# Kernel optimization log

Measured on AMD Instinct MI355X. Metric: run time of the kernel, lower is better.

The kernel has to match this reference:

```python
import jax, jax.numpy as jnp
import numpy as np

IN_Q = 256   # in_features // 4
OUT_Q = 256  # out_features // 4


def setup_inputs() -> dict:
    key = jax.random.key(0)
    kx, kr, ki, kj, kk = jax.random.split(key, 5)
    stdv = 1.0 / np.sqrt(IN_Q)
    return {
        "x": jax.random.normal(kx, (4, 8192, IN_Q * 4), dtype=jnp.float32),
        "r_weight": jax.random.uniform(kr, (OUT_Q, IN_Q), minval=-stdv, maxval=stdv, dtype=jnp.float32),
        "i_weight": jax.random.uniform(ki, (OUT_Q, IN_Q), minval=-stdv, maxval=stdv, dtype=jnp.float32),
        "j_weight": jax.random.uniform(kj, (OUT_Q, IN_Q), minval=-stdv, maxval=stdv, dtype=jnp.float32),
        "k_weight": jax.random.uniform(kk, (OUT_Q, IN_Q), minval=-stdv, maxval=stdv, dtype=jnp.float32),
        "bias": jnp.zeros((OUT_Q * 4,), dtype=jnp.float32),
    }


def reference(x, r_weight, i_weight, j_weight, k_weight, bias):
    batch_dims = x.shape[:-1]
    xq = x.reshape(*batch_dims, IN_Q, 4)  # [..., in_q, 4]
    r_x, i_x, j_x, k_x = xq[..., 0], xq[..., 1], xq[..., 2], xq[..., 3]

    lin = lambda v, w: jnp.einsum('...i,oi->...o', v, w)  # F.linear, no bias

    out_r = lin(r_x, r_weight) - lin(i_x, i_weight) - lin(j_x, j_weight) - lin(k_x, k_weight)
    out_i = lin(r_x, i_weight) + lin(i_x, r_weight) + lin(j_x, k_weight) - lin(k_x, j_weight)
    out_j = lin(r_x, j_weight) - lin(i_x, k_weight) + lin(j_x, r_weight) + lin(k_x, i_weight)
    out_k = lin(r_x, k_weight) + lin(i_x, j_weight) - lin(j_x, i_weight) + lin(k_x, r_weight)

    out = jnp.stack([out_r, out_i, out_j, out_k], axis=-1)  # [..., out_q, 4]
    out = out.reshape(*batch_dims, OUT_Q * 4)
    return out + bias
```

## Files before the change

kernel.cpp:

```cpp
#include <hip/hip_runtime.h>


typedef __attribute__((ext_vector_type(8))) short bf16x8;
typedef __attribute__((ext_vector_type(4))) float f32x4;

#define M_TOT 32768
#define N_TOT 1024
#define K_TOT 1024
#define BM 128
#define BN 128
#define BK 32

__device__ __forceinline__ unsigned short f2bf(float f) {
    union { float f; unsigned int u; } v; v.f = f;
    unsigned int u = v.u;
    u += 0x7fffu + ((u >> 16) & 1u);
    return (unsigned short)(u >> 16);
}

__global__ __launch_bounds__(256) void cvt_x(const float4* __restrict__ x,
                                             ushort4* __restrict__ y) {
    int idx = blockIdx.x * 256 + threadIdx.x;
    float4 a = x[idx];
    ushort4 o;
    o.x = f2bf(a.x); o.y = f2bf(a.y); o.z = f2bf(a.z); o.w = f2bf(a.w);
    y[idx] = o;
}

__global__ __launch_bounds__(256) void build_w(const float* __restrict__ R,
                                               const float* __restrict__ I,
                                               const float* __restrict__ J,
                                               const float* __restrict__ Kw,
                                               ushort4* __restrict__ Wb) {
    int n = blockIdx.x;
    int i = threadIdx.x;
    int o = n >> 2, co = n & 3;
    int base = o * 256 + i;
    float r = R[base], ii = I[base], j = J[base], k = Kw[base];
    float v0, v1, v2, v3;
    if (co == 0)      { v0 = r;  v1 = -ii; v2 = -j;  v3 = -k; }
    else if (co == 1) { v0 = ii; v1 = r;   v2 = k;   v3 = -j; }
    else if (co == 2) { v0 = j;  v1 = -k;  v2 = r;   v3 = ii; }
    else              { v0 = k;  v1 = j;   v2 = -ii; v3 = r;  }
    ushort4 w;
    w.x = f2bf(v0); w.y = f2bf(v1); w.z = f2bf(v2); w.w = f2bf(v3);
    Wb[n * 256 + i] = w;
}

__device__ __forceinline__ void async_lds16(const void* g, void* l) {
    __builtin_amdgcn_global_load_lds(
        (const __attribute__((address_space(1))) unsigned int*)g,
        (__attribute__((address_space(3))) unsigned int*)l,
        16, 0, 0);
}

__global__ __launch_bounds__(256) void gemm_bt(
        const unsigned short* __restrict__ A,
        const unsigned short* __restrict__ B,
        const float* __restrict__ bias,
        float* __restrict__ C) {
    __shared__ unsigned short As[BM * BK];
    __shared__ unsigned short Bs[BN * BK];

    const int tid  = threadIdx.x;
    const int wave = tid >> 6;
    const int lane = tid & 63;
    const int quad = lane >> 4;
    const int r16  = lane & 15;
    const int wm   = wave & 1;
    const int wn   = wave >> 1;

    const int m0 = blockIdx.x * BM;
    const int n0 = blockIdx.y * BN;

    f32x4 acc[4][4];
#pragma unroll
    for (int i = 0; i < 4; ++i)
#pragma unroll
        for (int j = 0; j < 4; ++j)
            acc[i][j] = (f32x4){0.f, 0.f, 0.f, 0.f};

    const int srow = lane >> 2;
    const int scol = (lane & 3) * 8;

    for (int k0 = 0; k0 < K_TOT; k0 += BK) {
        __syncthreads();
#pragma unroll
        for (int j = 0; j < 2; ++j) {
            int q   = wave * 2 + j;
            int row = q * 16 + srow;
            async_lds16(A + (size_t)(m0 + row) * K_TOT + k0 + scol, As + q * 512);
            async_lds16(B + (size_t)(n0 + row) * K_TOT + k0 + scol, Bs + q * 512);
        }
        __syncthreads();

        bf16x8 af[4], bf[4];
#pragma unroll
        for (int i = 0; i < 4; ++i) {
            af[i] = *(const bf16x8*)(As + (wm * 64 + i * 16 + r16) * BK + quad * 8);
            bf[i] = *(const bf16x8*)(Bs + (wn * 64 + i * 16 + r16) * BK + quad * 8);
        }
#pragma unroll
        for (int i = 0; i < 4; ++i)
#pragma unroll
            for (int j = 0; j < 4; ++j)
                acc[i][j] = __builtin_amdgcn_mfma_f32_16x16x32_bf16(
                    af[i], bf[j], acc[i][j], 0, 0, 0);
    }

#pragma unroll
    for (int j = 0; j < 4; ++j) {
        int col  = n0 + wn * 64 + j * 16 + r16;
        float bv = bias[col];
#pragma unroll
        for (int i = 0; i < 4; ++i) {
            int rowb = m0 + wm * 64 + i * 16 + quad * 4;
            f32x4 v  = acc[i][j];
#pragma unroll
            for (int r = 0; r < 4; ++r)
                C[(size_t)(rowb + r) * N_TOT + col] = v[r] + bv;
        }
    }
}

extern "C" void kernel_launch(void* const* d_in, const int* in_sizes, int n_in,
                              void* d_out, int out_size, void* d_ws, size_t ws_size,
                              hipStream_t stream) {
    const float* x    = (const float*)d_in[0];
    const float* rw   = (const float*)d_in[1];
    const float* iw   = (const float*)d_in[2];
    const float* jw   = (const float*)d_in[3];
    const float* kw   = (const float*)d_in[4];
    const float* bias = (const float*)d_in[5];
    float* out = (float*)d_out;

    unsigned short* xb = (unsigned short*)d_ws;
    unsigned short* Wb = (unsigned short*)((char*)d_ws + (size_t)M_TOT * K_TOT * 2);

    cvt_x<<<(M_TOT * (size_t)K_TOT) / 4 / 256, 256, 0, stream>>>(
        (const float4*)x, (ushort4*)xb);

    build_w<<<N_TOT, 256, 0, stream>>>(rw, iw, jw, kw, (ushort4*)Wb);

    dim3 grid(M_TOT / BM, N_TOT / BN);
    gemm_bt<<<grid, 256, 0, stream>>>(xb, Wb, bias, out);
}
```

Baseline: 329.2 us.

## Fuse fp32-to-bf16 conversion of x into GEMM A-tile loading

Removes the separate cvt_x pass: the GEMM now loads fp32 x tiles directly into registers, converts them to bf16, and writes them to LDS, while B still uses async global-to-LDS loads. The grid is reordered so the N-tiles of one M-block run adjacently, letting the repeated fp32 A reads hit in cache. This avoids writing and re-reading a 64MB bf16 copy of x. In exchange, A traffic per tile doubles in bytes, and the synchronous register-path loads plus conversion add latency inside the main loop.

```diff
diff --git a/kernel.cpp b/kernel.cpp
--- a/kernel.cpp
+++ b/kernel.cpp
@@ -16,15 +16,6 @@
     unsigned int u = v.u;
     u += 0x7fffu + ((u >> 16) & 1u);
     return (unsigned short)(u >> 16);
-}
-
-__global__ __launch_bounds__(256) void cvt_x(const float4* __restrict__ x,
-                                             ushort4* __restrict__ y) {
-    int idx = blockIdx.x * 256 + threadIdx.x;
-    float4 a = x[idx];
-    ushort4 o;
-    o.x = f2bf(a.x); o.y = f2bf(a.y); o.z = f2bf(a.z); o.w = f2bf(a.w);
-    y[idx] = o;
 }
 
 __global__ __launch_bounds__(256) void build_w(const float* __restrict__ R,
@@ -54,8 +45,8 @@
         16, 0, 0);
 }
 
-__global__ __launch_bounds__(256) void gemm_bt(
-        const unsigned short* __restrict__ A,
+__global__ __launch_bounds__(256) void gemm_fused(
+        const float* __restrict__ A,
         const unsigned short* __restrict__ B,
         const float* __restrict__ bias,
         float* __restrict__ C) {
@@ -70,8 +61,8 @@
     const int wm   = wave & 1;
     const int wn   = wave >> 1;
 
-    const int m0 = blockIdx.x * BM;
-    const int n0 = blockIdx.y * BN;
+    const int n0 = blockIdx.x * BN;
+    const int m0 = blockIdx.y * BM;
 
     f32x4 acc[4][4];
 #pragma unroll
@@ -83,15 +74,33 @@
     const int srow = lane >> 2;
     const int scol = (lane & 3) * 8;
 
+    const int arow0 = tid >> 3;
+    const int acol  = (tid & 7) * 4;
+
     for (int k0 = 0; k0 < K_TOT; k0 += BK) {
+        float4 av[4];
+#pragma unroll
+        for (int c = 0; c < 4; ++c)
+            av[c] = *(const float4*)(A + (size_t)(m0 + arow0 + c * 32) * K_TOT
+                                       + k0 + acol);
+
         __syncthreads();
+
 #pragma unroll
         for (int j = 0; j < 2; ++j) {
             int q   = wave * 2 + j;
             int row = q * 16 + srow;
-            async_lds16(A + (size_t)(m0 + row) * K_TOT + k0 + scol, As + q * 512);
             async_lds16(B + (size_t)(n0 + row) * K_TOT + k0 + scol, Bs + q * 512);
         }
+
+#pragma unroll
+        for (int c = 0; c < 4; ++c) {
+            ushort4 uv;
+            uv.x = f2bf(av[c].x); uv.y = f2bf(av[c].y);
+            uv.z = f2bf(av[c].z); uv.w = f2bf(av[c].w);
+            *(ushort4*)(As + (arow0 + c * 32) * BK + acol) = uv;
+        }
+
         __syncthreads();
 
         bf16x8 af[4], bf[4];
@@ -134,14 +143,10 @@
     const float* bias = (const float*)d_in[5];
     float* out = (float*)d_out;
 
-    unsigned short* xb = (unsigned short*)d_ws;
-    unsigned short* Wb = (unsigned short*)((char*)d_ws + (size_t)M_TOT * K_TOT * 2);
-
-    cvt_x<<<(M_TOT * (size_t)K_TOT) / 4 / 256, 256, 0, stream>>>(
-        (const float4*)x, (ushort4*)xb);
+    unsigned short* Wb = (unsigned short*)d_ws;
 
     build_w<<<N_TOT, 256, 0, stream>>>(rw, iw, jw, kw, (ushort4*)Wb);
 
-    dim3 grid(M_TOT / BM, N_TOT / BN);
-    gemm_bt<<<grid, 256, 0, stream>>>(xb, Wb, bias, out);
+    dim3 grid(N_TOT / BN, M_TOT / BM);
+    gemm_fused<<<grid, 256, 0, stream>>>(x, Wb, bias, out);
 }
```

After: 354.6 us. 1.08x slower.
